# Kernel optimization log

Hardware: AMD Instinct MI355X
Metric: run time of the kernel (lower is better)

The kernel has to match this reference:

```python
import jax, jax.numpy as jnp
import numpy as np

LAMBDA_ATTENTION = 0.33
LAMBDA_DISTANCE = 0.33
LAMBDA_ADJACENCY = 1.0 - LAMBDA_ATTENTION - LAMBDA_DISTANCE
EPS = 1e-06
NEG_INF = 1000000000000.0


def setup_inputs() -> dict:
    key = jax.random.key(0)
    kq, kk, kv, ka, kd = jax.random.split(key, 5)
    B, H, S, D = 16, 16, 512, 64
    return {
        "query": jax.random.normal(kq, (B, H, S, D), dtype=jnp.float32),
        "key": jax.random.normal(kk, (B, H, S, D), dtype=jnp.float32),
        "value": jax.random.normal(kv, (B, H, S, D), dtype=jnp.float32),
        "mask": jnp.ones((B, 1, S), dtype=jnp.float32),
        "adj_matrix": jax.random.uniform(ka, (B, S, S), dtype=jnp.float32),
        "distance_matrix": jax.random.uniform(kd, (B, S, S), dtype=jnp.float32),
    }


def reference(query, key, value, mask, adj_matrix, distance_matrix):
    d_k = query.shape[-1]
    # scores: [B,H,S,S]
    scores = jnp.einsum("bhqd,bhkd->bhqk", query, key) / jnp.sqrt(jnp.asarray(d_k, query.dtype))
    # mask [B,1,S] -> broadcast to [B,H,S,S] over key axis
    key_mask = mask[:, :, None, :]  # [B,1,1,S]
    scores = jnp.where(key_mask == 0, -NEG_INF, scores)
    p_attn = jax.nn.softmax(scores, axis=-1)

    # row-normalized adjacency, broadcast over heads
    adj_norm = adj_matrix / (jnp.sum(adj_matrix, axis=-1, keepdims=True) + EPS)  # [B,S,S]

    # distance kernel: mask key positions with +inf then softmax(-x)
    dist = jnp.where(mask == 0, jnp.inf, distance_matrix)  # mask [B,1,S] broadcasts over rows
    p_dist = jax.nn.softmax(-dist, axis=-1)  # [B,S,S]

    p_weighted = (LAMBDA_ATTENTION * p_attn
                  + LAMBDA_DISTANCE * p_dist[:, None, :, :]
                  + LAMBDA_ADJACENCY * adj_norm[:, None, :, :])
    # dropout is identity in eval mode
    out = jnp.einsum("bhqk,bhkd->bhqd", p_weighted, value)
    return out, p_attn
```

## Files before the change

### kernel.cpp

```cpp
#include <hip/hip_runtime.h>
#include <cmath>

#define BATCH 16
#define HEADS 16
#define SEQ   512
#define DIM   64
#define QT    32
#define NCHUNK 8

#define LAMBDA_A 0.33f
#define LAMBDA_D 0.33f
#define LAMBDA_J 0.34f
#define NEG_BIG  1.0e12f

typedef float  floatx4 __attribute__((ext_vector_type(4)));
typedef short  shortx8 __attribute__((ext_vector_type(8)));
typedef short  shortx4 __attribute__((ext_vector_type(4)));

__device__ __forceinline__ unsigned short f2bf(float x){
  unsigned u = __builtin_bit_cast(unsigned, x);
  u += 0x7FFFu + ((u >> 16) & 1u);
  return (unsigned short)(u >> 16);
}

__global__ __launch_bounds__(64) void stats_kernel(const float* __restrict__ mask,
                                                   const float* __restrict__ adj,
                                                   const float* __restrict__ dist,
                                                   float* __restrict__ ws){
  int bid  = blockIdx.x;
  int b    = bid >> 9;
  int lane = threadIdx.x;
  const float* arow = adj  + (size_t)bid * SEQ;
  const float* drow = dist + (size_t)bid * SEQ;
  const float* mrow = mask + b * SEQ;

  float asum = 0.f, dmax = -INFINITY;
  float xs[8];
#pragma unroll
  for (int i = 0; i < 8; i++){
    int n = lane + i * 64;
    asum += arow[n];
    float mk = mrow[n];
    float x  = (mk == 0.f) ? -INFINITY : -drow[n];
    xs[i] = x;
    dmax  = fmaxf(dmax, x);
  }
#pragma unroll
  for (int off = 1; off < 64; off <<= 1){
    asum += __shfl_xor(asum, off);
    dmax  = fmaxf(dmax, __shfl_xor(dmax, off));
  }
  float lsum = 0.f;
#pragma unroll
  for (int i = 0; i < 8; i++) lsum += __expf(xs[i] - dmax);
#pragma unroll
  for (int off = 1; off < 64; off <<= 1) lsum += __shfl_xor(lsum, off);

  if (lane == 0){
    ws[bid]             = 1.f / (asum + 1e-6f);
    ws[8192  + bid]     = dmax;
    ws[16384 + bid]     = 1.f / lsum;
  }
}

__global__ __launch_bounds__(256, 3) void attn_kernel(
    const float* __restrict__ Q, const float* __restrict__ K, const float* __restrict__ V,
    const float* __restrict__ mask, const float* __restrict__ adj, const float* __restrict__ dist,
    const float* __restrict__ ws, float* __restrict__ out, float* __restrict__ pattn){

  int bx  = blockIdx.x;
  int qt  = bx & 15;
  int bh  = bx >> 4;
  int b   = bh >> 4;
  int q0  = qt * QT;

  int tid  = threadIdx.x;
  int wave = tid >> 6;
  int lane = tid & 63;
  int l15  = lane & 15;
  int quad = lane >> 4;

  __shared__ short sQ [32 * 72];
  __shared__ short sKV[64 * 72];
  __shared__ short sPW[32 * 520];
  __shared__ float sMask[SEQ];
  __shared__ float sRedM[2][32];
  __shared__ float sRedS[2][32];

  const float* Qb = Q + ((size_t)bh * SEQ + q0) * DIM;
  const float* Kb = K + (size_t)bh * SEQ * DIM;
  const float* Vb = V + (size_t)bh * SEQ * DIM;

#pragma unroll
  for (int i = 0; i < 2; i++){
    int f = i * 1024 + tid * 4;
    floatx4 v = *(const floatx4*)(Qb + f);
    int row = f >> 6, col = f & 63;
    shortx4 h;
    h[0] = (short)f2bf(v[0] * 0.125f);
    h[1] = (short)f2bf(v[1] * 0.125f);
    h[2] = (short)f2bf(v[2] * 0.125f);
    h[3] = (short)f2bf(v[3] * 0.125f);
    *(shortx4*)&sQ[row * 72 + col] = h;
  }
  sMask[tid]       = mask[b * SEQ + tid];
  sMask[tid + 256] = mask[b * SEQ + tid + 256];

  int mtile = wave & 1;
  int p     = wave >> 1;

  floatx4 acc[16];
#pragma unroll
  for (int j = 0; j < 16; j++) acc[j] = (floatx4)0.f;

  for (int c = 0; c < NCHUNK; c++){
    if (c) __syncthreads();
    const float* Kc = Kb + c * 64 * DIM;
#pragma unroll
    for (int i = 0; i < 4; i++){
      int f = i * 1024 + tid * 4;
      floatx4 v = *(const floatx4*)(Kc + f);
      int row = f >> 6, col = f & 63;
      shortx4 h;
      h[0] = (short)f2bf(v[0]);
      h[1] = (short)f2bf(v[1]);
      h[2] = (short)f2bf(v[2]);
      h[3] = (short)f2bf(v[3]);
      *(shortx4*)&sKV[row * 72 + col] = h;
    }
    __syncthreads();
#pragma unroll
    for (int ks = 0; ks < 2; ks++){
      shortx8 af = *(const shortx8*)&sQ[(mtile * 16 + l15) * 72 + ks * 32 + quad * 8];
      shortx8 b0 = *(const shortx8*)&sKV[(p * 16 + l15) * 72 + ks * 32 + quad * 8];
      acc[2 * c] = __builtin_amdgcn_mfma_f32_16x16x32_bf16(af, b0, acc[2 * c], 0, 0, 0);
      shortx8 b1 = *(const shortx8*)&sKV[((p + 2) * 16 + l15) * 72 + ks * 32 + quad * 8];
      acc[2 * c + 1] = __builtin_amdgcn_mfma_f32_16x16x32_bf16(af, b1, acc[2 * c + 1], 0, 0, 0);
    }
  }

  float vmax[4] = {-INFINITY, -INFINITY, -INFINITY, -INFINITY};
#pragma unroll
  for (int j = 0; j < 16; j++){
    int n = (2 * j + p) * 16 + l15;
    bool msk0 = (sMask[n] == 0.f);
#pragma unroll
    for (int r = 0; r < 4; r++){
      float s = msk0 ? -NEG_BIG : acc[j][r];
      acc[j][r] = s;
      vmax[r] = fmaxf(vmax[r], s);
    }
  }
#pragma unroll
  for (int r = 0; r < 4; r++){
#pragma unroll
    for (int off = 1; off < 16; off <<= 1)
      vmax[r] = fmaxf(vmax[r], __shfl_xor(vmax[r], off));
  }
  if (l15 == 0){
#pragma unroll
    for (int r = 0; r < 4; r++) sRedM[p][mtile * 16 + quad * 4 + r] = vmax[r];
  }
  __syncthreads();
  float mrow[4];
#pragma unroll
  for (int r = 0; r < 4; r++){
    int ridx = mtile * 16 + quad * 4 + r;
    mrow[r] = fmaxf(sRedM[0][ridx], sRedM[1][ridx]);
  }
  float vsum[4] = {0.f, 0.f, 0.f, 0.f};
#pragma unroll
  for (int j = 0; j < 16; j++){
#pragma unroll
    for (int r = 0; r < 4; r++){
      float e = __expf(acc[j][r] - mrow[r]);
      acc[j][r] = e;
      vsum[r] += e;
    }
  }
#pragma unroll
  for (int r = 0; r < 4; r++){
#pragma unroll
    for (int off = 1; off < 16; off <<= 1)
      vsum[r] += __shfl_xor(vsum[r], off);
  }
  if (l15 == 0){
#pragma unroll
    for (int r = 0; r < 4; r++) sRedS[p][mtile * 16 + quad * 4 + r] = vsum[r];
  }
  __syncthreads();
  float inv_l[4];
#pragma unroll
  for (int r = 0; r < 4; r++){
    int ridx = mtile * 16 + quad * 4 + r;
    inv_l[r] = 1.f / (sRedS[0][ridx] + sRedS[1][ridx]);
  }

  float* pA = pattn + ((size_t)bh * SEQ + q0) * SEQ;
  const float* arow_base = adj  + ((size_t)b * SEQ + q0) * SEQ;
  const float* drow_base = dist + ((size_t)b * SEQ + q0) * SEQ;
  const float* iadj = ws;
  const float* mds  = ws + 8192;
  const float* ils  = ws + 16384;

#pragma unroll
  for (int r = 0; r < 4; r++){
    int rl = mtile * 16 + quad * 4 + r;
    int qg = b * SEQ + q0 + rl;
    float ia = iadj[qg];
    float md = mds[qg];
    float il = ils[qg];
#pragma unroll
    for (int j = 0; j < 16; j++){
      int n = (2 * j + p) * 16 + l15;
      float pa = acc[j][r] * inv_l[r];
      __builtin_nontemporal_store(pa, &pA[(size_t)rl * SEQ + n]);
      float a  = arow_base[(size_t)rl * SEQ + n];
      float dd = drow_base[(size_t)rl * SEQ + n];
      float mk = sMask[n];
      float pd = (mk == 0.f) ? 0.f : __expf(-dd - md) * il;
      float pw = LAMBDA_A * pa + LAMBDA_D * pd + LAMBDA_J * a * ia;
      sPW[rl * 520 + n] = (short)f2bf(pw);
    }
  }
  __syncthreads();

  floatx4 acc2[2];
  acc2[0] = (floatx4)0.f;
  acc2[1] = (floatx4)0.f;
  int mtile2 = wave & 1;
  int p2     = wave >> 1;

  for (int c = 0; c < NCHUNK; c++){
    if (c) __syncthreads();
    {
      int n = tid & 63, g = tid >> 6;
      const float* Vc = Vb + c * 64 * DIM;
      shortx8 w0, w1;
#pragma unroll
      for (int i = 0; i < 8; i++)  w0[i] = (short)f2bf(Vc[(g * 16 + i) * DIM + n]);
#pragma unroll
      for (int i = 0; i < 8; i++)  w1[i] = (short)f2bf(Vc[(g * 16 + 8 + i) * DIM + n]);
      *(shortx8*)&sKV[n * 72 + g * 16]     = w0;
      *(shortx8*)&sKV[n * 72 + g * 16 + 8] = w1;
    }
    __syncthreads();
#pragma unroll
    for (int ks = 0; ks < 2; ks++){
      shortx8 af = *(const shortx8*)&sPW[(mtile2 * 16 + l15) * 520 + c * 64 + ks * 32 + quad * 8];
      shortx8 b0 = *(const shortx8*)&sKV[(p2 * 16 + l15) * 72 + ks * 32 + quad * 8];
      acc2[0] = __builtin_amdgcn_mfma_f32_16x16x32_bf16(af, b0, acc2[0], 0, 0, 0);
      shortx8 b1 = *(const shortx8*)&sKV[((p2 + 2) * 16 + l15) * 72 + ks * 32 + quad * 8];
      acc2[1] = __builtin_amdgcn_mfma_f32_16x16x32_bf16(af, b1, acc2[1], 0, 0, 0);
    }
  }

  float* ob = out + ((size_t)bh * SEQ + q0) * DIM;
#pragma unroll
  for (int t = 0; t < 2; t++){
    int nt = p2 + 2 * t;
#pragma unroll
    for (int r = 0; r < 4; r++){
      int rl = mtile2 * 16 + quad * 4 + r;
      __builtin_nontemporal_store(acc2[t][r], &ob[(size_t)rl * DIM + nt * 16 + l15]);
    }
  }
}

extern "C" void kernel_launch(void* const* d_in, const int* in_sizes, int n_in,
                              void* d_out, int out_size, void* d_ws, size_t ws_size,
                              hipStream_t stream){
  const float* Q    = (const float*)d_in[0];
  const float* K    = (const float*)d_in[1];
  const float* V    = (const float*)d_in[2];
  const float* mask = (const float*)d_in[3];
  const float* adj  = (const float*)d_in[4];
  const float* dist = (const float*)d_in[5];
  float* out   = (float*)d_out;
  float* pattn = out + (size_t)BATCH * HEADS * SEQ * DIM;
  float* ws    = (float*)d_ws;

  stats_kernel<<<BATCH * SEQ, 64, 0, stream>>>(mask, adj, dist, ws);
  attn_kernel<<<BATCH * HEADS * (SEQ / QT), 256, 0, stream>>>(Q, K, V, mask, adj, dist,
                                                              ws, out, pattn);
}
```

Baseline: 591.1 us.

## Fuse row stats into attention kernel and interleave P-weight build with PV chunks

```diff
diff --git a/kernel.cpp b/kernel.cpp
--- a/kernel.cpp
+++ b/kernel.cpp
@@ -23,55 +23,17 @@
   return (unsigned short)(u >> 16);
 }
 
-__global__ __launch_bounds__(64) void stats_kernel(const float* __restrict__ mask,
-                                                   const float* __restrict__ adj,
-                                                   const float* __restrict__ dist,
-                                                   float* __restrict__ ws){
-  int bid  = blockIdx.x;
-  int b    = bid >> 9;
-  int lane = threadIdx.x;
-  const float* arow = adj  + (size_t)bid * SEQ;
-  const float* drow = dist + (size_t)bid * SEQ;
-  const float* mrow = mask + b * SEQ;
-
-  float asum = 0.f, dmax = -INFINITY;
-  float xs[8];
-#pragma unroll
-  for (int i = 0; i < 8; i++){
-    int n = lane + i * 64;
-    asum += arow[n];
-    float mk = mrow[n];
-    float x  = (mk == 0.f) ? -INFINITY : -drow[n];
-    xs[i] = x;
-    dmax  = fmaxf(dmax, x);
-  }
-#pragma unroll
-  for (int off = 1; off < 64; off <<= 1){
-    asum += __shfl_xor(asum, off);
-    dmax  = fmaxf(dmax, __shfl_xor(dmax, off));
-  }
-  float lsum = 0.f;
-#pragma unroll
-  for (int i = 0; i < 8; i++) lsum += __expf(xs[i] - dmax);
-#pragma unroll
-  for (int off = 1; off < 64; off <<= 1) lsum += __shfl_xor(lsum, off);
-
-  if (lane == 0){
-    ws[bid]             = 1.f / (asum + 1e-6f);
-    ws[8192  + bid]     = dmax;
-    ws[16384 + bid]     = 1.f / lsum;
-  }
-}
-
-__global__ __launch_bounds__(256, 3) void attn_kernel(
+__global__ __launch_bounds__(256, 4) void attn_kernel(
     const float* __restrict__ Q, const float* __restrict__ K, const float* __restrict__ V,
     const float* __restrict__ mask, const float* __restrict__ adj, const float* __restrict__ dist,
-    const float* __restrict__ ws, float* __restrict__ out, float* __restrict__ pattn){
+    float* __restrict__ out, float* __restrict__ pattn){
 
   int bx  = blockIdx.x;
-  int qt  = bx & 15;
-  int bh  = bx >> 4;
-  int b   = bh >> 4;
+  int h   = bx & 15;
+  int rest= bx >> 4;
+  int qt  = rest & 15;
+  int b   = rest >> 4;
+  int bh  = b * HEADS + h;
   int q0  = qt * QT;
 
   int tid  = threadIdx.x;
@@ -82,10 +44,12 @@
 
   __shared__ short sQ [32 * 72];
   __shared__ short sKV[64 * 72];
-  __shared__ short sPW[32 * 520];
+  __shared__ short sPW[32 * 72];
   __shared__ float sMask[SEQ];
   __shared__ float sRedM[2][32];
   __shared__ float sRedS[2][32];
+  __shared__ float sRowA[32];
+  __shared__ float sRowD[32];
 
   const float* Qb = Q + ((size_t)bh * SEQ + q0) * DIM;
   const float* Kb = K + (size_t)bh * SEQ * DIM;
@@ -96,15 +60,45 @@
     int f = i * 1024 + tid * 4;
     floatx4 v = *(const floatx4*)(Qb + f);
     int row = f >> 6, col = f & 63;
-    shortx4 h;
-    h[0] = (short)f2bf(v[0] * 0.125f);
-    h[1] = (short)f2bf(v[1] * 0.125f);
-    h[2] = (short)f2bf(v[2] * 0.125f);
-    h[3] = (short)f2bf(v[3] * 0.125f);
-    *(shortx4*)&sQ[row * 72 + col] = h;
+    shortx4 hh;
+    hh[0] = (short)f2bf(v[0] * 0.125f);
+    hh[1] = (short)f2bf(v[1] * 0.125f);
+    hh[2] = (short)f2bf(v[2] * 0.125f);
+    hh[3] = (short)f2bf(v[3] * 0.125f);
+    *(shortx4*)&sQ[row * 72 + col] = hh;
   }
   sMask[tid]       = mask[b * SEQ + tid];
   sMask[tid + 256] = mask[b * SEQ + tid + 256];
+  __syncthreads();
+
+  {
+    int rl  = tid >> 3;
+    int sub = tid & 7;
+    const float* arow = adj  + ((size_t)b * SEQ + q0 + rl) * SEQ;
+    const float* drow = dist + ((size_t)b * SEQ + q0 + rl) * SEQ;
+    float asum = 0.f, dsum = 0.f;
+#pragma unroll
+    for (int k = 0; k < 16; k++){
+      int c4 = (k * 8 + sub) * 4;
+      floatx4 a4 = *(const floatx4*)(arow + c4);
+      floatx4 d4 = *(const floatx4*)(drow + c4);
+      asum += (a4[0] + a4[1]) + (a4[2] + a4[3]);
+#pragma unroll
+      for (int i = 0; i < 4; i++){
+        float mk = sMask[c4 + i];
+        dsum += (mk == 0.f) ? 0.f : __expf(-d4[i]);
+      }
+    }
+#pragma unroll
+    for (int off = 1; off < 8; off <<= 1){
+      asum += __shfl_xor(asum, off);
+      dsum += __shfl_xor(dsum, off);
+    }
+    if (sub == 0){
+      sRowA[rl] = 1.f / (asum + 1e-6f);
+      sRowD[rl] = 1.f / dsum;
+    }
+  }
 
   int mtile = wave & 1;
   int p     = wave >> 1;
@@ -121,12 +115,12 @@
       int f = i * 1024 + tid * 4;
       floatx4 v = *(const floatx4*)(Kc + f);
       int row = f >> 6, col = f & 63;
-      shortx4 h;
-      h[0] = (short)f2bf(v[0]);
-      h[1] = (short)f2bf(v[1]);
-      h[2] = (short)f2bf(v[2]);
-      h[3] = (short)f2bf(v[3]);
-      *(shortx4*)&sKV[row * 72 + col] = h;
+      shortx4 hh;
+      hh[0] = (short)f2bf(v[0]);
+      hh[1] = (short)f2bf(v[1]);
+      hh[2] = (short)f2bf(v[2]);
+      hh[3] = (short)f2bf(v[3]);
+      *(shortx4*)&sKV[row * 72 + col] = hh;
     }
     __syncthreads();
 #pragma unroll
@@ -199,37 +193,10 @@
   float* pA = pattn + ((size_t)bh * SEQ + q0) * SEQ;
   const float* arow_base = adj  + ((size_t)b * SEQ + q0) * SEQ;
   const float* drow_base = dist + ((size_t)b * SEQ + q0) * SEQ;
-  const float* iadj = ws;
-  const float* mds  = ws + 8192;
-  const float* ils  = ws + 16384;
-
-#pragma unroll
-  for (int r = 0; r < 4; r++){
-    int rl = mtile * 16 + quad * 4 + r;
-    int qg = b * SEQ + q0 + rl;
-    float ia = iadj[qg];
-    float md = mds[qg];
-    float il = ils[qg];
-#pragma unroll
-    for (int j = 0; j < 16; j++){
-      int n = (2 * j + p) * 16 + l15;
-      float pa = acc[j][r] * inv_l[r];
-      __builtin_nontemporal_store(pa, &pA[(size_t)rl * SEQ + n]);
-      float a  = arow_base[(size_t)rl * SEQ + n];
-      float dd = drow_base[(size_t)rl * SEQ + n];
-      float mk = sMask[n];
-      float pd = (mk == 0.f) ? 0.f : __expf(-dd - md) * il;
-      float pw = LAMBDA_A * pa + LAMBDA_D * pd + LAMBDA_J * a * ia;
-      sPW[rl * 520 + n] = (short)f2bf(pw);
-    }
-  }
-  __syncthreads();
 
   floatx4 acc2[2];
   acc2[0] = (floatx4)0.f;
   acc2[1] = (floatx4)0.f;
-  int mtile2 = wave & 1;
-  int p2     = wave >> 1;
 
   for (int c = 0; c < NCHUNK; c++){
     if (c) __syncthreads();
@@ -244,13 +211,32 @@
       *(shortx8*)&sKV[n * 72 + g * 16]     = w0;
       *(shortx8*)&sKV[n * 72 + g * 16 + 8] = w1;
     }
+#pragma unroll
+    for (int r = 0; r < 4; r++){
+      int rl = mtile * 16 + quad * 4 + r;
+      float ia = sRowA[rl];
+      float il = sRowD[rl];
+#pragma unroll
+      for (int jj = 0; jj < 2; jj++){
+        int nloc = (2 * jj + p) * 16 + l15;
+        int n    = c * 64 + nloc;
+        float pa = acc[2 * c + jj][r] * inv_l[r];
+        __builtin_nontemporal_store(pa, &pA[(size_t)rl * SEQ + n]);
+        float a  = arow_base[(size_t)rl * SEQ + n];
+        float dd = drow_base[(size_t)rl * SEQ + n];
+        float mk = sMask[n];
+        float pd = (mk == 0.f) ? 0.f : __expf(-dd) * il;
+        float pw = LAMBDA_A * pa + LAMBDA_D * pd + LAMBDA_J * a * ia;
+        sPW[rl * 72 + nloc] = (short)f2bf(pw);
+      }
+    }
     __syncthreads();
 #pragma unroll
     for (int ks = 0; ks < 2; ks++){
-      shortx8 af = *(const shortx8*)&sPW[(mtile2 * 16 + l15) * 520 + c * 64 + ks * 32 + quad * 8];
-      shortx8 b0 = *(const shortx8*)&sKV[(p2 * 16 + l15) * 72 + ks * 32 + quad * 8];
+      shortx8 af = *(const shortx8*)&sPW[(mtile * 16 + l15) * 72 + ks * 32 + quad * 8];
+      shortx8 b0 = *(const shortx8*)&sKV[(p * 16 + l15) * 72 + ks * 32 + quad * 8];
       acc2[0] = __builtin_amdgcn_mfma_f32_16x16x32_bf16(af, b0, acc2[0], 0, 0, 0);
-      shortx8 b1 = *(const shortx8*)&sKV[((p2 + 2) * 16 + l15) * 72 + ks * 32 + quad * 8];
+      shortx8 b1 = *(const shortx8*)&sKV[((p + 2) * 16 + l15) * 72 + ks * 32 + quad * 8];
       acc2[1] = __builtin_amdgcn_mfma_f32_16x16x32_bf16(af, b1, acc2[1], 0, 0, 0);
     }
   }
@@ -258,10 +244,10 @@
   float* ob = out + ((size_t)bh * SEQ + q0) * DIM;
 #pragma unroll
   for (int t = 0; t < 2; t++){
-    int nt = p2 + 2 * t;
-#pragma unroll
-    for (int r = 0; r < 4; r++){
-      int rl = mtile2 * 16 + quad * 4 + r;
+    int nt = p + 2 * t;
+#pragma unroll
+    for (int r = 0; r < 4; r++){
+      int rl = mtile * 16 + quad * 4 + r;
       __builtin_nontemporal_store(acc2[t][r], &ob[(size_t)rl * DIM + nt * 16 + l15]);
     }
   }
@@ -278,9 +264,7 @@
   const float* dist = (const float*)d_in[5];
   float* out   = (float*)d_out;
   float* pattn = out + (size_t)BATCH * HEADS * SEQ * DIM;
-  float* ws    = (float*)d_ws;
-
-  stats_kernel<<<BATCH * SEQ, 64, 0, stream>>>(mask, adj, dist, ws);
+
   attn_kernel<<<BATCH * HEADS * (SEQ / QT), 256, 0, stream>>>(Q, K, V, mask, adj, dist,
-                                                              ws, out, pattn);
+                                                              out, pattn);
 }
```

Result: faster. 565.2 us (-4.4%).
